# Kernel tuning notes

Hardware: AMD Instinct MI355X
Metric: run time of the kernel (lower is better)

Reference implementation:

```python
import math
import jax, jax.numpy as jnp
import numpy as np

D = 128
R = 64
BETA = 1.0


def setup_inputs() -> dict:
    key = jax.random.key(0)
    k1, k2 = jax.random.split(key)
    X_tilde = jax.random.normal(k1, (8, 2048, D), dtype=jnp.float32)
    W = jax.random.normal(k2, (D, R), dtype=jnp.float32) / math.sqrt(R)
    return {"X_tilde": X_tilde, "W": W}


def reference(X_tilde, W):
    # S = W W^T / sqrt(d*r), shape (d, d)
    d, r = W.shape
    S = (W @ W.T) / math.sqrt(d * r)
    B, T, _ = X_tilde.shape
    # gram = X S X^T, shape (B, T, T)
    XS = jnp.einsum('btd,de->bte', X_tilde, S)
    gram = jnp.einsum('bte,bse->bts', XS, X_tilde)
    # trace-centering: subtract (tr(gram)/T) * I
    trace = jnp.einsum('btt->b', gram)  # (B,)
    eye = jnp.eye(T, dtype=X_tilde.dtype)
    centered = gram - (trace / T)[:, None, None] * eye[None, :, :]
    scores = centered / math.sqrt(d)  # normalize_sqrt_d=True
    A = jax.nn.softmax(BETA * scores, axis=-1)  # (B, T, T)
    Y_hat = jnp.einsum('bts,bsd->btd', A, X_tilde)
    return Y_hat
```

## Files before the change

### kernel.cpp

```cpp
#include <hip/hip_runtime.h>
#include <hip/hip_bf16.h>
#include <math.h>

#define D_DIM 128
#define R_DIM 64
#define T_DIM 2048
#define B_DIM 8
#define NS 4
#define SCHUNK (T_DIM / NS)
#define SBLK 64
#define NIT (SCHUNK / SBLK)
#define KE_CONST (0.08838834764831845f * 1.4426950408889634f)

typedef __attribute__((ext_vector_type(8))) short bf16x8;
typedef __attribute__((ext_vector_type(4))) short s16x4;
typedef __attribute__((ext_vector_type(4))) float f32x4;
typedef __attribute__((ext_vector_type(16))) float f32x16;

__device__ inline unsigned short f2bf(float f) {
  union { float f; unsigned int u; } v; v.f = f;
  return (unsigned short)((v.u + 0x7FFFu + ((v.u >> 16) & 1u)) >> 16);
}
__device__ inline float bf2f(unsigned short u) {
  union { unsigned int u; float f; } v; v.u = ((unsigned int)u) << 16;
  return v.f;
}
__device__ inline unsigned int cvt_pk_bf16(float lo, float hi) {
  unsigned int r;
  asm("v_cvt_pk_bf16_f32 %0, %1, %2" : "=v"(r) : "v"(lo), "v"(hi));
  return r;
}
__device__ inline void permswap(unsigned int& a, unsigned int& b) {
  asm("v_permlane32_swap_b32 %0, %1" : "+v"(a), "+v"(b));
}
__device__ inline float fexp2(float x) {
  float r;
  asm("v_exp_f32 %0, %1" : "=v"(r) : "v"(x));
  return r;
}

__device__ inline void async16(const short* l, const unsigned short* g) {
  __builtin_amdgcn_global_load_lds(
      (const __attribute__((address_space(1))) unsigned int*)g,
      (__attribute__((address_space(3))) unsigned int*)l, 16, 0, 0);
}

__global__ void k_s(const float* __restrict__ W, unsigned short* __restrict__ Sb) {
  int gid = blockIdx.x * 256 + threadIdx.x;
  int i = gid >> 7, j = gid & 127;
  const float* wi = W + i * R_DIM;
  const float* wj = W + j * R_DIM;
  float acc = 0.f;
#pragma unroll 8
  for (int r = 0; r < R_DIM; ++r) acc += wi[r] * wj[r];
  int off = (((i >> 4) * 4 + (j >> 5)) * 64 + ((j & 31) >> 3) * 16 + (i & 15)) * 8 + (j & 7);
  Sb[off] = f2bf(acc * 0.011048543456039806f);
}

__global__ void __launch_bounds__(128) k_prep(
    const float* __restrict__ X, const unsigned short* __restrict__ Sb,
    unsigned short* __restrict__ Qb, unsigned short* __restrict__ Xb,
    unsigned short* __restrict__ Xt, float* __restrict__ part) {
  const int tid = threadIdx.x;
  const int w = tid >> 6, lane = tid & 63;
  const int g = lane >> 4, c = lane & 15;
  const int b = blockIdx.y;
  const int t0 = blockIdx.x * 16;

  __shared__ __align__(16) short xbT[D_DIM * 16];
  __shared__ __align__(16) float accLds[8 * 64 * 4];

  union FU { unsigned int wd[4]; bf16x8 v; };
  bf16x8 xf[2];
#pragma unroll
  for (int kcl = 0; kcl < 2; ++kcl) {
    const int kc = w * 2 + kcl;
    const float* xp = X + ((size_t)(b * T_DIM + t0 + c)) * D_DIM + kc * 32 + g * 8;
    f32x4 a = *(const f32x4*)xp;
    f32x4 bb = *(const f32x4*)(xp + 4);
    FU f;
    f.wd[0] = cvt_pk_bf16(a[0], a[1]);
    f.wd[1] = cvt_pk_bf16(a[2], a[3]);
    f.wd[2] = cvt_pk_bf16(bb[0], bb[1]);
    f.wd[3] = cvt_pk_bf16(bb[2], bb[3]);
    xf[kcl] = f.v;
    *(bf16x8*)(Xb + ((size_t)(b * T_DIM + t0 + c)) * D_DIM + kc * 32 + g * 8) = f.v;
#pragma unroll
    for (int jw = 0; jw < 4; ++jw) {
      unsigned int wv = f.wd[jw];
      int e = kc * 32 + g * 8 + jw * 2;
      xbT[(e + 0) * 16 + c] = (short)wv;
      xbT[(e + 1) * 16 + c] = (short)(wv >> 16);
    }
  }

  f32x4 acc[8];
#pragma unroll
  for (int dc = 0; dc < 8; ++dc) acc[dc] = (f32x4){0.f, 0.f, 0.f, 0.f};
#pragma unroll
  for (int dc = 0; dc < 8; ++dc) {
    bf16x8 sf[2];
#pragma unroll
    for (int kcl = 0; kcl < 2; ++kcl)
      sf[kcl] = *(const bf16x8*)(Sb + ((size_t)(dc * 4 + w * 2 + kcl) * 64 + lane) * 8);
#pragma unroll
    for (int kcl = 0; kcl < 2; ++kcl)
      acc[dc] = __builtin_amdgcn_mfma_f32_16x16x32_bf16(xf[kcl], sf[kcl], acc[dc], 0, 0, 0);
  }

  if (w == 1) {
#pragma unroll
    for (int dc = 0; dc < 8; ++dc)
#pragma unroll
      for (int r = 0; r < 4; ++r)
        accLds[dc * 256 + lane * 4 + r] = acc[dc][r];
  }
  __syncthreads();

  if (w == 0) {
    float trp = 0.f;
#pragma unroll
    for (int dc = 0; dc < 8; ++dc)
#pragma unroll
      for (int r = 0; r < 4; ++r) {
        float q = acc[dc][r] + accLds[dc * 256 + lane * 4 + r];
        float x = bf2f((unsigned short)xbT[(dc * 16 + c) * 16 + g * 4 + r]);
        trp += q * x;
        int t = t0 + g * 4 + r;
        size_t qoff = (((size_t)(b * 64 + (t >> 5)) * 8 + dc) * 512 +
                       ((c >> 3) * 32 + (t & 31)) * 8 + (c & 7));
        Qb[qoff] = (unsigned short)cvt_pk_bf16(q * KE_CONST, 0.f);
      }
    trp += __shfl_xor(trp, 1); trp += __shfl_xor(trp, 2);
    trp += __shfl_xor(trp, 4); trp += __shfl_xor(trp, 8);
    trp += __shfl_xor(trp, 16); trp += __shfl_xor(trp, 32);
    if (lane == 0) part[b * 128 + blockIdx.x] = trp;
  }

#pragma unroll
  for (int p = 0; p < 2; ++p) {
    int row = p * 64 + (tid >> 1);
    bf16x8 v = *(const bf16x8*)&xbT[row * 16 + (tid & 1) * 8];
    *(bf16x8*)(Xt + ((size_t)(b * D_DIM + row)) * T_DIM + t0 + (tid & 1) * 8) = v;
  }
}

__global__ void __launch_bounds__(256, 2) k_attn(
    const unsigned short* __restrict__ Qb, const unsigned short* __restrict__ Xb,
    const unsigned short* __restrict__ Xt, const float* __restrict__ part,
    unsigned short* __restrict__ accp, float* __restrict__ rsp) {
  const int tid = threadIdx.x;
  const int wave = tid >> 6, lane = tid & 63;
  const int tl = lane & 31;
  const int h = lane >> 5;
  const int lin = blockIdx.x;
  const int b = lin & 7;
  const int kk = lin >> 3;
  const int ns = kk & 3;
  const int tile = kk >> 2;
  const int t0w = tile * 128 + wave * 32;

  const unsigned short* Xbb = Xb + (size_t)b * T_DIM * D_DIM;
  const unsigned short* Xtb = Xt + (size_t)b * D_DIM * T_DIM;

  float tv = part[b * 128 + lane] + part[b * 128 + 64 + lane];
  tv += __shfl_xor(tv, 1); tv += __shfl_xor(tv, 2);
  tv += __shfl_xor(tv, 4); tv += __shfl_xor(tv, 8);
  tv += __shfl_xor(tv, 16); tv += __shfl_xor(tv, 32);
  const float ctrK = tv * (1.0f / T_DIM) * KE_CONST;
  const float expCtr = fexp2(-ctrK);

  __shared__ __align__(16) short sKs[2][SBLK * D_DIM];
  __shared__ __align__(16) short sVs[2][D_DIM * SBLK];

  int oK[8];
#pragma unroll
  for (int kc = 0; kc < 8; ++kc)
    oK[kc] = tl * 128 + (((kc * 2 + h) ^ (tl & 15)) * 8);

  const unsigned short* qbase =
      Qb + ((size_t)(b * 64 + tile * 4 + wave)) * 8 * 512;
  bf16x8 qf[8];
#pragma unroll
  for (int kc = 0; kc < 8; ++kc)
    qf[kc] = *(const bf16x8*)(qbase + (size_t)kc * 512 + lane * 8);

  f32x16 acc[4];
#pragma unroll
  for (int dt = 0; dt < 4; ++dt)
#pragma unroll
    for (int r = 0; r < 16; ++r) acc[dt][r] = 0.f;
  float denacc = 0.f;

  const int s_beg = ns * SCHUNK;

  auto stage = [&](int buf, int sb) {
#pragma unroll
    for (int q = 0; q < 4; ++q) {
      int j = wave * 256 + q * 64 + lane;
      int row = j >> 4, sc = j & 15;
      int lc = sc ^ (row & 15);
      async16(&sKs[buf][(wave * 256 + q * 64) * 8],
              Xbb + (size_t)(sb + row) * D_DIM + lc * 8);
    }
#pragma unroll
    for (int q = 0; q < 4; ++q) {
      int j = wave * 256 + q * 64 + lane;
      int row = j >> 3, sc = j & 7;
      int lc = sc ^ (row & 7);
      async16(&sVs[buf][(wave * 256 + q * 64) * 8],
              Xtb + (size_t)row * T_DIM + sb + lc * 8);
    }
  };

  stage(0, s_beg);

  for (int it = 0; it < NIT; ++it) {
    const int buf = it & 1;
    const int sb = s_beg + it * SBLK;

    if (it < NIT - 1) {
      stage(buf ^ 1, sb + SBLK);
      asm volatile("s_waitcnt vmcnt(8)" ::: "memory");
    } else {
      asm volatile("s_waitcnt vmcnt(0)" ::: "memory");
    }
    __builtin_amdgcn_sched_barrier(0);
    __builtin_amdgcn_s_barrier();

    const short* kb = &sKs[buf][0];
    const short* vb = &sVs[buf][0];

#pragma unroll
    for (int sub = 0; sub < 2; ++sub) {
      bf16x8 kf[8];
#pragma unroll
      for (int kc = 0; kc < 8; ++kc)
        kf[kc] = *(const bf16x8*)(kb + sub * 32 * 128 + oK[kc]);
      bf16x8 vf[4][2];
#pragma unroll
      for (int dt = 0; dt < 4; ++dt)
#pragma unroll
        for (int sck = 0; sck < 2; ++sck)
          vf[dt][sck] = *(const bf16x8*)(vb + (dt * 32 + tl) * 64 +
                                         (((sub * 4 + sck * 2 + h) ^ (tl & 7)) * 8));

      f32x16 sa, sb2;
#pragma unroll
      for (int r = 0; r < 16; ++r) { sa[r] = 0.f; sb2[r] = 0.f; }
#pragma unroll
      for (int kc = 0; kc < 4; ++kc) {
        sa  = __builtin_amdgcn_mfma_f32_32x32x16_bf16(kf[kc],     qf[kc],     sa,  0, 0, 0);
        sb2 = __builtin_amdgcn_mfma_f32_32x32x16_bf16(kf[kc + 4], qf[kc + 4], sb2, 0, 0, 0);
      }
      f32x16 sc = sa + sb2;

      const bool isd = (sb + sub * 32 == t0w);

#pragma unroll
      for (int sck = 0; sck < 2; ++sck) {
        float p[8];
#pragma unroll
        for (int q = 0; q < 8; ++q) p[q] = fexp2(sc[sck * 8 + q]);
        if (isd) {
#pragma unroll
          for (int q = 0; q < 8; ++q) {
            int rowid = (q & 3) + 8 * (q >> 2) + 16 * sck + 4 * h;
            if (rowid == tl) p[q] *= expCtr;
          }
        }
#pragma unroll
        for (int q = 0; q < 8; ++q) denacc += p[q];
        unsigned int W0 = cvt_pk_bf16(p[0], p[1]);
        unsigned int W1 = cvt_pk_bf16(p[2], p[3]);
        unsigned int W2 = cvt_pk_bf16(p[4], p[5]);
        unsigned int W3 = cvt_pk_bf16(p[6], p[7]);
        permswap(W0, W2);
        permswap(W1, W3);
        union PU { unsigned int wd[4]; bf16x8 v; } pu;
        pu.wd[0] = W0; pu.wd[1] = W1; pu.wd[2] = W2; pu.wd[3] = W3;
#pragma unroll
        for (int dt = 0; dt < 4; ++dt)
          acc[dt] = __builtin_amdgcn_mfma_f32_32x32x16_bf16(pu.v, vf[dt][sck],
                                                            acc[dt], 0, 0, 0);
      }
    }

    __builtin_amdgcn_s_barrier();
  }

  float den = denacc + __shfl_xor(denacc, 32);
  if (lane < 32)
    rsp[(b * NS + ns) * T_DIM + t0w + lane] = den;

  const size_t pbase = ((size_t)(b * NS + ns)) * T_DIM * D_DIM;
#pragma unroll
  for (int dt = 0; dt < 4; ++dt)
#pragma unroll
    for (int r = 0; r < 16; ++r) {
      int rowid = (r & 3) + 8 * (r >> 2) + 4 * h;
      accp[pbase + (size_t)(t0w + rowid) * D_DIM + dt * 32 + tl] =
          (unsigned short)cvt_pk_bf16(acc[dt][r], 0.f);
    }
}

__global__ void __launch_bounds__(256) k_comb(
    const unsigned short* __restrict__ accp, const float* __restrict__ rsp,
    float* __restrict__ out) {
  const int lin = blockIdx.x;
  const int b = lin & 7;
  const int kk = lin >> 3;
  int ib = kk * 2048 + threadIdx.x * 8;
  int d = ib & 127;
  int t = ib >> 7;
  float num[8] = {0.f, 0.f, 0.f, 0.f, 0.f, 0.f, 0.f, 0.f};
  float den = 0.f;
#pragma unroll
  for (int ns = 0; ns < NS; ++ns) {
    const unsigned short* p =
        accp + (((size_t)(b * NS + ns)) * T_DIM + t) * D_DIM + d;
    bf16x8 v = *(const bf16x8*)p;
#pragma unroll
    for (int j = 0; j < 8; ++j) num[j] += bf2f((unsigned short)v[j]);
    den += rsp[(b * NS + ns) * T_DIM + t];
  }
  float inv = 1.0f / den;
  float* o = out + ((size_t)b * T_DIM * D_DIM + ib);
  f32x4 o0 = (f32x4){num[0] * inv, num[1] * inv, num[2] * inv, num[3] * inv};
  f32x4 o1 = (f32x4){num[4] * inv, num[5] * inv, num[6] * inv, num[7] * inv};
  *(f32x4*)(o + 0) = o0;
  *(f32x4*)(o + 4) = o1;
}

extern "C" void kernel_launch(void* const* d_in, const int* in_sizes, int n_in,
                              void* d_out, int out_size, void* d_ws, size_t ws_size,
                              hipStream_t stream) {
  const float* X = (const float*)d_in[0];
  const float* W = (const float*)d_in[1];
  float* out = (float*)d_out;
  char* ws = (char*)d_ws;

  unsigned short* Sb = (unsigned short*)(ws);
  float* part        = (float*)(ws + 32768);
  unsigned short* Qb = (unsigned short*)(ws + 65536);
  unsigned short* Xb = (unsigned short*)(ws + 65536 + 4194304);
  unsigned short* Xt = (unsigned short*)(ws + 65536 + 2 * 4194304);
  unsigned short* accp = (unsigned short*)(ws + 65536 + 3 * 4194304);
  float* rsp         = (float*)(ws + 65536 + 3 * 4194304 + 16777216);

  k_s<<<64, 256, 0, stream>>>(W, Sb);
  k_prep<<<dim3(T_DIM / 16, B_DIM), 128, 0, stream>>>(X, Sb, Qb, Xb, Xt, part);
  k_attn<<<(T_DIM / 128) * NS * B_DIM, 256, 0, stream>>>(Qb, Xb, Xt, part, accp, rsp);
  k_comb<<<B_DIM * 128, 256, 0, stream>>>(accp, rsp, out);
}
```

Baseline: 43.60 us.

## Fuse split-K combine into attention kernel via last-arriver atomic counter

Removes the separate combine kernel launch by having the last of the NS split blocks for each (batch, tile) reduce the partial numerators and denominators and write the final output. Arrival is detected with an atomic counter per tile, reset in k_s, with threadfences for visibility. This saves a kernel launch and its dependency gap. In exchange, the final reduction is serialized onto 128 tail blocks and some extra fence and atomic overhead is added.

Result: slower. 114.2 us (+162.0%).

```diff
diff --git a/kernel.cpp b/kernel.cpp
--- a/kernel.cpp
+++ b/kernel.cpp
@@ -13,7 +13,6 @@
 #define KE_CONST (0.08838834764831845f * 1.4426950408889634f)
 
 typedef __attribute__((ext_vector_type(8))) short bf16x8;
-typedef __attribute__((ext_vector_type(4))) short s16x4;
 typedef __attribute__((ext_vector_type(4))) float f32x4;
 typedef __attribute__((ext_vector_type(16))) float f32x16;
 
@@ -45,8 +44,10 @@
       (__attribute__((address_space(3))) unsigned int*)l, 16, 0, 0);
 }
 
-__global__ void k_s(const float* __restrict__ W, unsigned short* __restrict__ Sb) {
+__global__ void k_s(const float* __restrict__ W, unsigned short* __restrict__ Sb,
+                    unsigned int* __restrict__ cnt) {
   int gid = blockIdx.x * 256 + threadIdx.x;
+  if (gid < 128) cnt[gid] = 0u;
   int i = gid >> 7, j = gid & 127;
   const float* wi = W + i * R_DIM;
   const float* wj = W + j * R_DIM;
@@ -148,7 +149,8 @@
 __global__ void __launch_bounds__(256, 2) k_attn(
     const unsigned short* __restrict__ Qb, const unsigned short* __restrict__ Xb,
     const unsigned short* __restrict__ Xt, const float* __restrict__ part,
-    unsigned short* __restrict__ accp, float* __restrict__ rsp) {
+    unsigned short* __restrict__ accp, float* __restrict__ rsp,
+    float* __restrict__ out, unsigned int* __restrict__ cnt) {
   const int tid = threadIdx.x;
   const int wave = tid >> 6, lane = tid & 63;
   const int tl = lane & 31;
@@ -172,6 +174,7 @@
 
   __shared__ __align__(16) short sKs[2][SBLK * D_DIM];
   __shared__ __align__(16) short sVs[2][D_DIM * SBLK];
+  __shared__ unsigned int arriveOrd;
 
   int oK[8];
 #pragma unroll
@@ -302,34 +305,36 @@
       accp[pbase + (size_t)(t0w + rowid) * D_DIM + dt * 32 + tl] =
           (unsigned short)cvt_pk_bf16(acc[dt][r], 0.f);
     }
-}
-
-__global__ void __launch_bounds__(256) k_comb(
-    const unsigned short* __restrict__ accp, const float* __restrict__ rsp,
-    float* __restrict__ out) {
-  const int lin = blockIdx.x;
-  const int b = lin & 7;
-  const int kk = lin >> 3;
-  int ib = kk * 2048 + threadIdx.x * 8;
-  int d = ib & 127;
-  int t = ib >> 7;
-  float num[8] = {0.f, 0.f, 0.f, 0.f, 0.f, 0.f, 0.f, 0.f};
-  float den = 0.f;
-#pragma unroll
-  for (int ns = 0; ns < NS; ++ns) {
-    const unsigned short* p =
-        accp + (((size_t)(b * NS + ns)) * T_DIM + t) * D_DIM + d;
-    bf16x8 v = *(const bf16x8*)p;
-#pragma unroll
-    for (int j = 0; j < 8; ++j) num[j] += bf2f((unsigned short)v[j]);
-    den += rsp[(b * NS + ns) * T_DIM + t];
-  }
-  float inv = 1.0f / den;
-  float* o = out + ((size_t)b * T_DIM * D_DIM + ib);
-  f32x4 o0 = (f32x4){num[0] * inv, num[1] * inv, num[2] * inv, num[3] * inv};
-  f32x4 o1 = (f32x4){num[4] * inv, num[5] * inv, num[6] * inv, num[7] * inv};
-  *(f32x4*)(o + 0) = o0;
-  *(f32x4*)(o + 4) = o1;
+
+  __threadfence();
+  if (tid == 0) arriveOrd = atomicAdd(&cnt[b * 16 + tile], 1u);
+  __syncthreads();
+  if (arriveOrd == NS - 1) {
+    __threadfence();
+#pragma unroll
+    for (int u = 0; u < 8; ++u) {
+      int ib = tile * 16384 + u * 2048 + tid * 8;
+      int d = ib & 127;
+      int t = ib >> 7;
+      float num[8] = {0.f, 0.f, 0.f, 0.f, 0.f, 0.f, 0.f, 0.f};
+      float den2 = 0.f;
+#pragma unroll
+      for (int n2 = 0; n2 < NS; ++n2) {
+        const unsigned short* p =
+            accp + (((size_t)(b * NS + n2)) * T_DIM + t) * D_DIM + d;
+        bf16x8 v = *(const bf16x8*)p;
+#pragma unroll
+        for (int j = 0; j < 8; ++j) num[j] += bf2f((unsigned short)v[j]);
+        den2 += rsp[(b * NS + n2) * T_DIM + t];
+      }
+      float inv = 1.0f / den2;
+      float* o = out + ((size_t)b * T_DIM * D_DIM + ib);
+      f32x4 o0 = (f32x4){num[0] * inv, num[1] * inv, num[2] * inv, num[3] * inv};
+      f32x4 o1 = (f32x4){num[4] * inv, num[5] * inv, num[6] * inv, num[7] * inv};
+      *(f32x4*)(o + 0) = o0;
+      *(f32x4*)(o + 4) = o1;
+    }
+  }
 }
 
 extern "C" void kernel_launch(void* const* d_in, const int* in_sizes, int n_in,
@@ -342,14 +347,15 @@
 
   unsigned short* Sb = (unsigned short*)(ws);
   float* part        = (float*)(ws + 32768);
+  unsigned int* cnt  = (unsigned int*)(ws + 40960);
   unsigned short* Qb = (unsigned short*)(ws + 65536);
   unsigned short* Xb = (unsigned short*)(ws + 65536 + 4194304);
   unsigned short* Xt = (unsigned short*)(ws + 65536 + 2 * 4194304);
   unsigned short* accp = (unsigned short*)(ws + 65536 + 3 * 4194304);
   float* rsp         = (float*)(ws + 65536 + 3 * 4194304 + 16777216);
 
-  k_s<<<64, 256, 0, stream>>>(W, Sb);
+  k_s<<<64, 256, 0, stream>>>(W, Sb, cnt);
   k_prep<<<dim3(T_DIM / 16, B_DIM), 128, 0, stream>>>(X, Sb, Qb, Xb, Xt, part);
-  k_attn<<<(T_DIM / 128) * NS * B_DIM, 256, 0, stream>>>(Qb, Xb, Xt, part, accp, rsp);
-  k_comb<<<B_DIM * 128, 256, 0, stream>>>(accp, rsp, out);
-}
+  k_attn<<<(T_DIM / 128) * NS * B_DIM, 256, 0, stream>>>(Qb, Xb, Xt, part, accp, rsp,
+                                                          out, cnt);
+}
```
